# Kernel optimization log

Hardware: AMD Instinct MI355X
Metric: run time of the kernel (lower is better)

Reference implementation:

```python
import jax, jax.numpy as jnp
from jax import lax
import numpy as np

B, N_VARS, M_CLAUSES, K_DIM = 1024, 64, 256, 12
MAX_ITER = 12


def setup_inputs() -> dict:
    key = jax.random.key(0)
    k1, k2, k3, k4 = jax.random.split(key, 4)
    z = jax.random.uniform(k1, (B, N_VARS), dtype=jnp.float32)          # input probabilities
    S = jax.random.normal(k2, (M_CLAUSES, N_VARS + 1), dtype=jnp.float32) * 0.2  # learnable clause matrix (col 0 = truth var)
    w = jax.random.uniform(k3, (M_CLAUSES,), dtype=jnp.float32)          # learnable clause weights
    r = jax.random.normal(k4, (B, N_VARS, K_DIM), dtype=jnp.float32)     # random init directions
    return {"z": z, "S": S, "w": w, "r": r, "max_iter": MAX_ITER}


def _mixing(z, S, w, r, max_iter):
    Bsz, n = z.shape
    m, N = S.shape  # N = n + 1 (truth variable is column 0)
    k = r.shape[-1]
    eps = jnp.float32(1e-8)

    # truth direction v_T = e_0
    vT = jnp.zeros((k,), dtype=z.dtype).at[0].set(1.0)

    # random unit directions orthogonal to v_T (zero out component along e_0)
    r_perp = r.at[..., 0].set(0.0)
    r_perp = r_perp / jnp.maximum(jnp.linalg.norm(r_perp, axis=-1, keepdims=True), eps)

    # SATNet init: v_i = -cos(pi z_i) v_T + sin(pi z_i) r_perp_i
    ang = jnp.pi * z
    Vvars = -jnp.cos(ang)[..., None] * vT + jnp.sin(ang)[..., None] * r_perp  # [B,n,k]
    V = jnp.concatenate([jnp.broadcast_to(vT, (Bsz, 1, k)), Vvars], axis=1)   # [B,N,k]

    Sw = S * w[:, None]                       # weighted clause matrix [m,N]
    W = jnp.einsum('mn,bnk->bmk', Sw, V)      # running product Sw @ V, [B,m,k]
    snrm = jnp.sum(Sw * Sw, axis=0)           # ||s_i||^2 per variable, [N]

    def coord_step(carry, i):
        V, W = carry
        s_i = Sw[:, i]                         # [m]
        v_old = V[:, i, :]                     # [B,k]
        g = jnp.einsum('bmk,m->bk', W, s_i) - snrm[i] * v_old
        v_new = -g / jnp.maximum(jnp.linalg.norm(g, axis=-1, keepdims=True), eps)
        W = W + (v_new - v_old)[:, None, :] * s_i[None, :, None]  # rank-1 update
        V = V.at[:, i, :].set(v_new)
        return (V, W), None

    def sweep(carry, _):
        carry, _ = lax.scan(coord_step, carry, jnp.arange(1, N))  # coordinate descent over variables
        return carry, None

    (V, _), _ = lax.scan(sweep, (V, W), None, length=max_iter)

    # output probabilities: z_i = arccos(-v_i . v_T) / pi
    cos = jnp.clip(-V[:, 1:, 0], -1.0 + 1e-6, 1.0 - 1e-6)
    return jnp.arccos(cos) / jnp.pi


def reference(z, S, w, r, max_iter):
    return _mixing(z, S, w, r, max_iter)
```

## Files before the change

### kernel.cpp

```cpp
#include <hip/hip_runtime.h>
#include <math.h>

#define BATCH 1024
#define NV    64
#define MC    256
#define KD    12
#define PI_F  3.14159265358979323846f

#define CBUF   4544
#define C0OFF  4352
#define DGAOFF 4416
#define DGBOFF 4480

typedef float f2 __attribute__((ext_vector_type(2)));
typedef float v4f __attribute__((ext_vector_type(4)));

template <int CTRL>
__device__ __forceinline__ float dpp_addf(float x) {
  int y = __builtin_amdgcn_update_dpp(0, __float_as_int(x), CTRL, 0xF, 0xF, true);
  return x + __int_as_float(y);
}
__device__ __forceinline__ float allreduce16(float x) {
  x = dpp_addf<0xB1>(x);
  x = dpp_addf<0x4E>(x);
  x = dpp_addf<0x124>(x);
  x = dpp_addf<0x128>(x);
  return x;
}
__device__ __forceinline__ float readlane63(float x) {
  return __int_as_float(__builtin_amdgcn_readlane(__float_as_int(x), 63));
}

__device__ __forceinline__ void pin(v4f& x) { asm volatile("" : "+v"(x)); }

__global__ void compute_C_kernel(const float* __restrict__ S,
                                 const float* __restrict__ w,
                                 float* __restrict__ Cg, int nsplit) {
  const int q = blockIdx.x;
  const int mc = blockIdx.y;
  const int j = threadIdx.x;
  if (j > NV) return;
  const int v = (q + 1) % 64 + 1;
  const int mlen = MC / nsplit;
  const int m0 = mc * mlen;
  float a0 = 0.f, a1 = 0.f, a2 = 0.f, a3 = 0.f;
  for (int m = m0; m < m0 + mlen; m += 4) {
    const float w0 = w[m], w1 = w[m + 1], w2 = w[m + 2], w3 = w[m + 3];
    a0 = fmaf(S[(m + 0) * (NV + 1) + v] * w0 * w0, S[(m + 0) * (NV + 1) + j], a0);
    a1 = fmaf(S[(m + 1) * (NV + 1) + v] * w1 * w1, S[(m + 1) * (NV + 1) + j], a1);
    a2 = fmaf(S[(m + 2) * (NV + 1) + v] * w2 * w2, S[(m + 2) * (NV + 1) + j], a2);
    a3 = fmaf(S[(m + 3) * (NV + 1) + v] * w3 * w3, S[(m + 3) * (NV + 1) + j], a3);
  }
  const float acc = (a0 + a1) + (a2 + a3);
  float* buf = Cg + mc * CBUF;
  const int p1 = (v == 1) ? 64 : (v - 1);
  const int p2 = (v == 1) ? 63 : (v == 2) ? 64 : (v - 2);
  if (j == 0) buf[C0OFF + q] = acc;
  if (j == p1) buf[DGAOFF + (v - 1)] = acc;
  if (j == p2) buf[DGBOFF + (v - 1)] = acc;
  if (j > 0) {
    const float st = (j == v || j == p1 || j == p2) ? 0.f : acc;
    buf[q * 68 + (j - 1)] = st;
  }
}

__global__ __launch_bounds__(256, 1) void mixing_kernel(
    const float* __restrict__ z, const float* __restrict__ r,
    const float* __restrict__ Cg, const int* __restrict__ max_iter_p,
    float* __restrict__ out, int nsplit) {
  __shared__ float Ls[CBUF];

  const int t = threadIdx.x;
  const int l = t & 63;
  const int kq = l >> 4;
  const int n16 = l & 15;
  const int b = blockIdx.x * 4 + (t >> 6);
  const int max_iter = max_iter_p[0];

  {
    const float4* src = (const float4*)Cg;
    float4* dst = (float4*)Ls;
    for (int idx = t; idx < CBUF / 4; idx += 256) {
      float4 a = src[idx];
      for (int u = 1; u < nsplit; ++u) {
        const float4 p = src[u * (CBUF / 4) + idx];
        a.x += p.x; a.y += p.y; a.z += p.z; a.w += p.w;
      }
      dst[idx] = a;
    }
  }

  const float row0 = (kq == 0) ? 1.f : 0.f;

  f2 V01[4];
  float V2[4];
  #pragma unroll
  for (int s = 0; s < 4; ++s) {
    const int n = 4 * n16 + s;
    const float zv = z[b * NV + n];
    float rp[3];
    float ssp = 0.f;
    #pragma unroll
    for (int j = 0; j < 3; ++j) {
      const int k = 3 * kq + j;
      rp[j] = (k == 0) ? 0.f : r[(b * NV + n) * KD + k];
      ssp = fmaf(rp[j], rp[j], ssp);
    }
    ssp += __shfl_xor(ssp, 16, 64);
    ssp += __shfl_xor(ssp, 32, 64);
    const float inv = 1.f / fmaxf(sqrtf(ssp), 1e-8f);
    float sn, cs;
    sincosf(PI_F * zv, &sn, &cs);
    float vv[3];
    #pragma unroll
    for (int j = 0; j < 3; ++j) {
      const int k = 3 * kq + j;
      vv[j] = (k == 0) ? -cs : sn * rp[j] * inv;
    }
    V01[s].x = vv[0];
    V01[s].y = vv[1];
    V2[s] = vv[2];
  }

  __syncthreads();

  f2 P01, vp1_01, vp2_01;
  float P2, vp1_2, vp2_2;

  {
    const v4f ce = *(const v4f*)&Ls[63 * 68 + 4 * n16];
    const float c0 = Ls[C0OFF + 63];
    f2 q01 = ce.x * V01[0];
    float q2 = ce.x * V2[0];
    q01 = __builtin_elementwise_fma((f2){ce.y, ce.y}, V01[1], q01);
    q2 = fmaf(ce.y, V2[1], q2);
    q01 = __builtin_elementwise_fma((f2){ce.z, ce.z}, V01[2], q01);
    q2 = fmaf(ce.z, V2[2], q2);
    q01 = __builtin_elementwise_fma((f2){ce.w, ce.w}, V01[3], q01);
    q2 = fmaf(ce.w, V2[3], q2);
    q01.x = allreduce16(q01.x);
    q01.y = allreduce16(q01.y);
    q2 = allreduce16(q2);
    q01.x = fmaf(row0, c0, q01.x);
    P01 = q01; P2 = q2;
    const int src = l | 15;
    vp1_01.x = __shfl(V01[3].x, src, 64);
    vp1_01.y = __shfl(V01[3].y, src, 64);
    vp1_2    = __shfl(V2[3],    src, 64);
    vp2_01.x = __shfl(V01[2].x, src, 64);
    vp2_01.y = __shfl(V01[2].y, src, 64);
    vp2_2    = __shfl(V2[2],    src, 64);
  }

  v4f cbA[4], cbB[4], c0A, c0B, daA, daB, dbA, dbB;

  auto prefetch = [&](v4f cb[4], v4f& c0b, v4f& dab, v4f& dbb, int g) {
    #pragma unroll
    for (int s = 0; s < 4; ++s) {
      cb[s] = *(const v4f*)&Ls[(4 * g + s) * 68 + 4 * n16];
      pin(cb[s]);
    }
    c0b = *(const v4f*)&Ls[C0OFF + 4 * g];
    dab = *(const v4f*)&Ls[DGAOFF + 4 * g];
    dbb = *(const v4f*)&Ls[DGBOFF + 4 * g];
    pin(c0b); pin(dab); pin(dbb);
  };

  auto do_group = [&](int ii, const v4f cb[4], const v4f& c0b,
                      const v4f& dab, const v4f& dbb) {
    const bool own  = (n16 == ii);
    const bool ownP = (n16 == ((ii + 15) & 15));
    #pragma unroll
    for (int s = 0; s < 4; ++s) {
      const v4f ce = cb[s];
      const float db = dbb[s], da = dab[s];

      f2 g01 = __builtin_elementwise_fma((f2){db, db}, vp2_01, P01);
      float g2 = fmaf(db, vp2_2, P2);
      g01 = __builtin_elementwise_fma((f2){da, da}, vp1_01, g01);
      g2 = fmaf(da, vp1_2, g2);

      f2 q01 = ce.x * V01[0];
      float q2 = ce.x * V2[0];
      q01 = __builtin_elementwise_fma((f2){ce.y, ce.y}, V01[1], q01);
      q2 = fmaf(ce.y, V2[1], q2);
      q01 = __builtin_elementwise_fma((f2){ce.z, ce.z}, V01[2], q01);
      q2 = fmaf(ce.z, V2[2], q2);
      q01 = __builtin_elementwise_fma((f2){ce.w, ce.w}, V01[3], q01);
      q2 = fmaf(ce.w, V2[3], q2);

      float n2p = g01.x * g01.x;
      n2p = fmaf(g01.y, g01.y, n2p);
      n2p = fmaf(g2, g2, n2p);

      n2p = dpp_addf<0x142>(n2p);
      q01.x = dpp_addf<0xB1>(q01.x);
      q01.y = dpp_addf<0xB1>(q01.y);
      q2 = dpp_addf<0xB1>(q2);
      n2p = dpp_addf<0x143>(n2p);
      q01.x = dpp_addf<0x4E>(q01.x);
      q01.y = dpp_addf<0x4E>(q01.y);
      q2 = dpp_addf<0x4E>(q2);
      const float n2 = readlane63(n2p);
      q01.x = dpp_addf<0x124>(q01.x);
      q01.y = dpp_addf<0x124>(q01.y);
      q2 = dpp_addf<0x124>(q2);
      const float inv = __builtin_amdgcn_rsqf(fmaxf(n2, 1e-16f));
      q01.x = dpp_addf<0x128>(q01.x);
      q01.y = dpp_addf<0x128>(q01.y);
      q2 = dpp_addf<0x128>(q2);
      const f2 vn01 = g01 * (f2){-inv, -inv};
      const float vn2 = -g2 * inv;
      q01.x = fmaf(row0, c0b[s], q01.x);

      if (s == 0) {
        V01[3].x = ownP ? vp1_01.x : V01[3].x;
        V01[3].y = ownP ? vp1_01.y : V01[3].y;
        V2[3]    = ownP ? vp1_2    : V2[3];
      } else {
        V01[s - 1].x = own ? vp1_01.x : V01[s - 1].x;
        V01[s - 1].y = own ? vp1_01.y : V01[s - 1].y;
        V2[s - 1]    = own ? vp1_2    : V2[s - 1];
      }

      vp2_01 = vp1_01; vp2_2 = vp1_2;
      vp1_01 = vn01;   vp1_2 = vn2;
      P01 = q01;       P2 = q2;
    }
  };

  prefetch(cbA, c0A, daA, dbA, 0);

  for (int it = 0; it < max_iter; ++it) {
    for (int ih = 0; ih < 8; ++ih) {
      prefetch(cbB, c0B, daB, dbB, 2 * ih + 1);
      do_group(2 * ih, cbA, c0A, daA, dbA);
      prefetch(cbA, c0A, daA, dbA, (2 * ih + 2) & 15);
      do_group(2 * ih + 1, cbB, c0B, daB, dbB);
    }
  }

  {
    const bool l15 = (n16 == 15);
    V01[3].x = l15 ? vp1_01.x : V01[3].x;
    V01[3].y = l15 ? vp1_01.y : V01[3].y;
    V2[3]    = l15 ? vp1_2    : V2[3];
  }

  if (kq == 0) {
    float4 o;
    float* op = &o.x;
    #pragma unroll
    for (int s = 0; s < 4; ++s) {
      float cv = -V01[s].x;
      cv = fminf(fmaxf(cv, -1.f + 1e-6f), 1.f - 1e-6f);
      op[s] = acosf(cv) * (1.f / PI_F);
    }
    ((float4*)(out + b * NV))[n16] = o;
  }
}

extern "C" void kernel_launch(void* const* d_in, const int* in_sizes, int n_in,
                              void* d_out, int out_size, void* d_ws, size_t ws_size,
                              hipStream_t stream) {
  const float* z = (const float*)d_in[0];
  const float* S = (const float*)d_in[1];
  const float* w = (const float*)d_in[2];
  const float* r = (const float*)d_in[3];
  const int* max_iter = (const int*)d_in[4];
  float* Cg = (float*)d_ws;

  const int nsplit = (ws_size >= (size_t)8 * CBUF * 4) ? 8
                   : (ws_size >= (size_t)4 * CBUF * 4) ? 4 : 1;
  compute_C_kernel<<<dim3(NV, nsplit), 128, 0, stream>>>(S, w, Cg, nsplit);
  mixing_kernel<<<BATCH / 4, 256, 0, stream>>>(z, r, Cg, max_iter,
                                               (float*)d_out, nsplit);
}
```

Measured before the change: 166.5 us.

## Remap wave lanes to one k-dim per lane group and unroll variable sweep

Changes the per-wave thread mapping. Each lane now holds one k-dimension (kk) for a quarter of the variables (jg), instead of three k-components for four variables. The C matrix layout in LDS is rearranged to match, and the reduction over variables shrinks to two DPP steps plus one norm reduction across lane groups. The 64-step coordinate sweep is fully unrolled with inline-asm ds_read_b128 prefetches three rows ahead, and the per-step scalars are fetched with readlane from registers. This should cut the VALU and DPP work per step, at the cost of code size and more fragile hand scheduling with manual waitcnt.

```diff
diff --git a/kernel.cpp b/kernel.cpp
--- a/kernel.cpp
+++ b/kernel.cpp
@@ -7,31 +7,36 @@
 #define KD    12
 #define PI_F  3.14159265358979323846f
 
-#define CBUF   4544
-#define C0OFF  4352
-#define DGAOFF 4416
-#define DGBOFF 4480
-
-typedef float f2 __attribute__((ext_vector_type(2)));
+#define C0OFF  4096
+#define DGAOFF 4160
+#define DGBOFF 4224
+#define CBUF   4288
+
+typedef float f2  __attribute__((ext_vector_type(2)));
 typedef float v4f __attribute__((ext_vector_type(4)));
+typedef __attribute__((address_space(3))) float lds_f;
 
 template <int CTRL>
 __device__ __forceinline__ float dpp_addf(float x) {
   int y = __builtin_amdgcn_update_dpp(0, __float_as_int(x), CTRL, 0xF, 0xF, true);
   return x + __int_as_float(y);
 }
-__device__ __forceinline__ float allreduce16(float x) {
-  x = dpp_addf<0xB1>(x);
-  x = dpp_addf<0x4E>(x);
-  x = dpp_addf<0x124>(x);
-  x = dpp_addf<0x128>(x);
-  return x;
+template <int CTRL>
+__device__ __forceinline__ float dpp_movf(float x) {
+  return __int_as_float(
+      __builtin_amdgcn_update_dpp(0, __float_as_int(x), CTRL, 0xF, 0xF, true));
 }
 __device__ __forceinline__ float readlane63(float x) {
   return __int_as_float(__builtin_amdgcn_readlane(__float_as_int(x), 63));
 }
-
-__device__ __forceinline__ void pin(v4f& x) { asm volatile("" : "+v"(x)); }
+__device__ __forceinline__ float rlane(float x, int i) {
+  return __int_as_float(__builtin_amdgcn_readlane(__float_as_int(x), i));
+}
+
+template <int IMM>
+__device__ __forceinline__ void dsr(v4f& d, unsigned base) {
+  asm volatile("ds_read_b128 %0, %1 offset:%2" : "=v"(d) : "v"(base), "i"(IMM));
+}
 
 __global__ void compute_C_kernel(const float* __restrict__ S,
                                  const float* __restrict__ w,
@@ -59,8 +64,9 @@
   if (j == p1) buf[DGAOFF + (v - 1)] = acc;
   if (j == p2) buf[DGBOFF + (v - 1)] = acc;
   if (j > 0) {
+    const int j0 = j - 1;
     const float st = (j == v || j == p1 || j == p2) ? 0.f : acc;
-    buf[q * 68 + (j - 1)] = st;
+    buf[q * 64 + (j0 & 3) * 16 + (j0 >> 2)] = st;
   }
 }
 
@@ -68,12 +74,12 @@
     const float* __restrict__ z, const float* __restrict__ r,
     const float* __restrict__ Cg, const int* __restrict__ max_iter_p,
     float* __restrict__ out, int nsplit) {
-  __shared__ float Ls[CBUF];
+  __shared__ __align__(16) float Ls[CBUF];
 
   const int t = threadIdx.x;
   const int l = t & 63;
-  const int kq = l >> 4;
-  const int n16 = l & 15;
+  const int jg = l & 3;
+  const int kk = l >> 2;
   const int b = blockIdx.x * 4 + (t >> 6);
   const int max_iter = max_iter_p[0];
 
@@ -90,173 +96,143 @@
     }
   }
 
-  const float row0 = (kq == 0) ? 1.f : 0.f;
-
-  f2 V01[4];
-  float V2[4];
+  const float my_e0 = (kk == 0) ? 1.f : 0.f;
+
+  f2 Vv[8];
   #pragma unroll
-  for (int s = 0; s < 4; ++s) {
-    const int n = 4 * n16 + s;
-    const float zv = z[b * NV + n];
-    float rp[3];
-    float ssp = 0.f;
+  for (int p = 0; p < 8; ++p) {
     #pragma unroll
-    for (int j = 0; j < 3; ++j) {
-      const int k = 3 * kq + j;
-      rp[j] = (k == 0) ? 0.f : r[(b * NV + n) * KD + k];
-      ssp = fmaf(rp[j], rp[j], ssp);
+    for (int h = 0; h < 2; ++h) {
+      const int j0 = jg + 8 * p + 4 * h;
+      const float zv = z[b * NV + j0];
+      float rp = 0.f;
+      if (kk >= 1 && kk < KD) rp = r[(b * NV + j0) * KD + kk];
+      float ssp = rp * rp;
+      ssp += __shfl_xor(ssp, 4, 64);
+      ssp += __shfl_xor(ssp, 8, 64);
+      ssp += __shfl_xor(ssp, 16, 64);
+      ssp += __shfl_xor(ssp, 32, 64);
+      const float inv = 1.f / fmaxf(sqrtf(ssp), 1e-8f);
+      const float sn = __builtin_amdgcn_sinf(0.5f * zv);
+      const float cs = __builtin_amdgcn_cosf(0.5f * zv);
+      const float vv = (kk == 0) ? -cs : sn * rp * inv;
+      if (h) Vv[p].y = vv; else Vv[p].x = vv;
     }
-    ssp += __shfl_xor(ssp, 16, 64);
-    ssp += __shfl_xor(ssp, 32, 64);
-    const float inv = 1.f / fmaxf(sqrtf(ssp), 1e-8f);
-    float sn, cs;
-    sincosf(PI_F * zv, &sn, &cs);
-    float vv[3];
-    #pragma unroll
-    for (int j = 0; j < 3; ++j) {
-      const int k = 3 * kq + j;
-      vv[j] = (k == 0) ? -cs : sn * rp[j] * inv;
+  }
+
+  __syncthreads();
+
+  const float t0v = Ls[C0OFF + l];
+  const float t1v = Ls[DGAOFF + l];
+  const float t2v = Ls[DGBOFF + l];
+
+  float P, vp1, vp2;
+
+  {
+    const int rb = 63 * 64 + jg * 16;
+    const v4f c0r = *(const v4f*)&Ls[rb + 0];
+    const v4f c1r = *(const v4f*)&Ls[rb + 4];
+    const v4f c2r = *(const v4f*)&Ls[rb + 8];
+    const v4f c3r = *(const v4f*)&Ls[rb + 12];
+    f2 qa = (f2){c0r.x, c0r.y} * Vv[0];
+    qa = __builtin_elementwise_fma((f2){c0r.z, c0r.w}, Vv[1], qa);
+    qa = __builtin_elementwise_fma((f2){c2r.x, c2r.y}, Vv[4], qa);
+    qa = __builtin_elementwise_fma((f2){c2r.z, c2r.w}, Vv[5], qa);
+    f2 qb = (f2){c1r.x, c1r.y} * Vv[2];
+    qb = __builtin_elementwise_fma((f2){c1r.z, c1r.w}, Vv[3], qb);
+    qb = __builtin_elementwise_fma((f2){c3r.x, c3r.y}, Vv[6], qb);
+    qb = __builtin_elementwise_fma((f2){c3r.z, c3r.w}, Vv[7], qb);
+    const f2 qs = qa + qb;
+    float q = qs.x + qs.y;
+    q = dpp_addf<0xB1>(q);
+    q = dpp_addf<0x4E>(q);
+    q = fmaf(my_e0, Ls[C0OFF + 63], q);
+    P = q;
+    vp1 = dpp_movf<0xFF>(Vv[7].y);
+    vp2 = dpp_movf<0xAA>(Vv[7].y);
+  }
+
+  const unsigned lbase = (unsigned)(unsigned long long)(lds_f*)&Ls[jg * 16];
+
+  v4f Rb[16];
+
+#define PFROW(R) \
+  dsr<((((R) & 63) * 256) + 0)>(Rb[(((R) & 3) * 4) + 0], lbase); \
+  dsr<((((R) & 63) * 256) + 16)>(Rb[(((R) & 3) * 4) + 1], lbase); \
+  dsr<((((R) & 63) * 256) + 32)>(Rb[(((R) & 3) * 4) + 2], lbase); \
+  dsr<((((R) & 63) * 256) + 48)>(Rb[(((R) & 3) * 4) + 3], lbase);
+
+#define STEPF(I) { \
+  constexpr int i_ = (I); \
+  constexpr int j0w_ = (i_ + 63) & 63; \
+  constexpr int p_ = j0w_ >> 3; \
+  constexpr int h_ = (j0w_ >> 2) & 1; \
+  constexpr int jgo_ = j0w_ & 3; \
+  constexpr int s_ = (i_ & 3) * 4; \
+   \
+  asm volatile("s_waitcnt lgkmcnt(8)" ::: "memory"); \
+  __builtin_amdgcn_sched_barrier(0); \
+  PFROW(i_ + 3) \
+  const float da_ = rlane(t1v, i_); \
+  const float db_ = rlane(t2v, i_); \
+  const float c0_ = rlane(t0v, i_); \
+  const float g_ = fmaf(da_, vp1, fmaf(db_, vp2, P)); \
+  float t_ = g_ * g_; \
+  f2 qa_ = (f2){Rb[s_ + 0].x, Rb[s_ + 0].y} * Vv[0]; \
+  qa_ = __builtin_elementwise_fma((f2){Rb[s_ + 0].z, Rb[s_ + 0].w}, Vv[1], qa_); \
+  t_ = dpp_addf<0x124>(t_); \
+  qa_ = __builtin_elementwise_fma((f2){Rb[s_ + 2].x, Rb[s_ + 2].y}, Vv[4], qa_); \
+  qa_ = __builtin_elementwise_fma((f2){Rb[s_ + 2].z, Rb[s_ + 2].w}, Vv[5], qa_); \
+  t_ = dpp_addf<0x128>(t_); \
+  f2 qb_ = (f2){Rb[s_ + 1].x, Rb[s_ + 1].y} * Vv[2]; \
+  qb_ = __builtin_elementwise_fma((f2){Rb[s_ + 1].z, Rb[s_ + 1].w}, Vv[3], qb_); \
+  t_ = dpp_addf<0x142>(t_); \
+  qb_ = __builtin_elementwise_fma((f2){Rb[s_ + 3].x, Rb[s_ + 3].y}, Vv[6], qb_); \
+  qb_ = __builtin_elementwise_fma((f2){Rb[s_ + 3].z, Rb[s_ + 3].w}, Vv[7], qb_); \
+  t_ = dpp_addf<0x143>(t_); \
+  const f2 qs_ = qa_ + qb_; \
+  float q_ = qs_.x + qs_.y; \
+  const float n2_ = readlane63(t_); \
+  const float inv_ = __builtin_amdgcn_rsqf(fmaxf(n2_, 1e-16f)); \
+  q_ = dpp_addf<0xB1>(q_); \
+  q_ = dpp_addf<0x4E>(q_); \
+  const float vn_ = -g_ * inv_; \
+  q_ = fmaf(my_e0, c0_, q_); \
+  if constexpr (h_) { Vv[p_].y = (jg == jgo_) ? vp1 : Vv[p_].y; } \
+  else              { Vv[p_].x = (jg == jgo_) ? vp1 : Vv[p_].x; } \
+  vp2 = vp1; vp1 = vn_; P = q_; \
+}
+
+#define S4(N) STEPF((N) + 0) STEPF((N) + 1) STEPF((N) + 2) STEPF((N) + 3)
+#define S16(N) S4((N) + 0) S4((N) + 4) S4((N) + 8) S4((N) + 12)
+
+  asm volatile("s_waitcnt lgkmcnt(0)" ::: "memory");
+  __builtin_amdgcn_sched_barrier(0);
+  PFROW(0) PFROW(1) PFROW(2)
+
+  #pragma unroll 1
+  for (int it = 0; it < max_iter; ++it) {
+    S16(0) S16(16) S16(32) S16(48)
+  }
+
+  Vv[7].y = (jg == 3) ? vp1 : Vv[7].y;
+
+  __syncthreads();
+  {
+    float* Lw = Ls + (t >> 6) * 64;
+    if (kk == 0) {
+      Lw[jg +  0] = Vv[0].x; Lw[jg +  4] = Vv[0].y;
+      Lw[jg +  8] = Vv[1].x; Lw[jg + 12] = Vv[1].y;
+      Lw[jg + 16] = Vv[2].x; Lw[jg + 20] = Vv[2].y;
+      Lw[jg + 24] = Vv[3].x; Lw[jg + 28] = Vv[3].y;
+      Lw[jg + 32] = Vv[4].x; Lw[jg + 36] = Vv[4].y;
+      Lw[jg + 40] = Vv[5].x; Lw[jg + 44] = Vv[5].y;
+      Lw[jg + 48] = Vv[6].x; Lw[jg + 52] = Vv[6].y;
+      Lw[jg + 56] = Vv[7].x; Lw[jg + 60] = Vv[7].y;
     }
-    V01[s].x = vv[0];
-    V01[s].y = vv[1];
-    V2[s] = vv[2];
-  }
-
-  __syncthreads();
-
-  f2 P01, vp1_01, vp2_01;
-  float P2, vp1_2, vp2_2;
-
-  {
-    const v4f ce = *(const v4f*)&Ls[63 * 68 + 4 * n16];
-    const float c0 = Ls[C0OFF + 63];
-    f2 q01 = ce.x * V01[0];
-    float q2 = ce.x * V2[0];
-    q01 = __builtin_elementwise_fma((f2){ce.y, ce.y}, V01[1], q01);
-    q2 = fmaf(ce.y, V2[1], q2);
-    q01 = __builtin_elementwise_fma((f2){ce.z, ce.z}, V01[2], q01);
-    q2 = fmaf(ce.z, V2[2], q2);
-    q01 = __builtin_elementwise_fma((f2){ce.w, ce.w}, V01[3], q01);
-    q2 = fmaf(ce.w, V2[3], q2);
-    q01.x = allreduce16(q01.x);
-    q01.y = allreduce16(q01.y);
-    q2 = allreduce16(q2);
-    q01.x = fmaf(row0, c0, q01.x);
-    P01 = q01; P2 = q2;
-    const int src = l | 15;
-    vp1_01.x = __shfl(V01[3].x, src, 64);
-    vp1_01.y = __shfl(V01[3].y, src, 64);
-    vp1_2    = __shfl(V2[3],    src, 64);
-    vp2_01.x = __shfl(V01[2].x, src, 64);
-    vp2_01.y = __shfl(V01[2].y, src, 64);
-    vp2_2    = __shfl(V2[2],    src, 64);
-  }
-
-  v4f cbA[4], cbB[4], c0A, c0B, daA, daB, dbA, dbB;
-
-  auto prefetch = [&](v4f cb[4], v4f& c0b, v4f& dab, v4f& dbb, int g) {
-    #pragma unroll
-    for (int s = 0; s < 4; ++s) {
-      cb[s] = *(const v4f*)&Ls[(4 * g + s) * 68 + 4 * n16];
-      pin(cb[s]);
-    }
-    c0b = *(const v4f*)&Ls[C0OFF + 4 * g];
-    dab = *(const v4f*)&Ls[DGAOFF + 4 * g];
-    dbb = *(const v4f*)&Ls[DGBOFF + 4 * g];
-    pin(c0b); pin(dab); pin(dbb);
-  };
-
-  auto do_group = [&](int ii, const v4f cb[4], const v4f& c0b,
-                      const v4f& dab, const v4f& dbb) {
-    const bool own  = (n16 == ii);
-    const bool ownP = (n16 == ((ii + 15) & 15));
-    #pragma unroll
-    for (int s = 0; s < 4; ++s) {
-      const v4f ce = cb[s];
-      const float db = dbb[s], da = dab[s];
-
-      f2 g01 = __builtin_elementwise_fma((f2){db, db}, vp2_01, P01);
-      float g2 = fmaf(db, vp2_2, P2);
-      g01 = __builtin_elementwise_fma((f2){da, da}, vp1_01, g01);
-      g2 = fmaf(da, vp1_2, g2);
-
-      f2 q01 = ce.x * V01[0];
-      float q2 = ce.x * V2[0];
-      q01 = __builtin_elementwise_fma((f2){ce.y, ce.y}, V01[1], q01);
-      q2 = fmaf(ce.y, V2[1], q2);
-      q01 = __builtin_elementwise_fma((f2){ce.z, ce.z}, V01[2], q01);
-      q2 = fmaf(ce.z, V2[2], q2);
-      q01 = __builtin_elementwise_fma((f2){ce.w, ce.w}, V01[3], q01);
-      q2 = fmaf(ce.w, V2[3], q2);
-
-      float n2p = g01.x * g01.x;
-      n2p = fmaf(g01.y, g01.y, n2p);
-      n2p = fmaf(g2, g2, n2p);
-
-      n2p = dpp_addf<0x142>(n2p);
-      q01.x = dpp_addf<0xB1>(q01.x);
-      q01.y = dpp_addf<0xB1>(q01.y);
-      q2 = dpp_addf<0xB1>(q2);
-      n2p = dpp_addf<0x143>(n2p);
-      q01.x = dpp_addf<0x4E>(q01.x);
-      q01.y = dpp_addf<0x4E>(q01.y);
-      q2 = dpp_addf<0x4E>(q2);
-      const float n2 = readlane63(n2p);
-      q01.x = dpp_addf<0x124>(q01.x);
-      q01.y = dpp_addf<0x124>(q01.y);
-      q2 = dpp_addf<0x124>(q2);
-      const float inv = __builtin_amdgcn_rsqf(fmaxf(n2, 1e-16f));
-      q01.x = dpp_addf<0x128>(q01.x);
-      q01.y = dpp_addf<0x128>(q01.y);
-      q2 = dpp_addf<0x128>(q2);
-      const f2 vn01 = g01 * (f2){-inv, -inv};
-      const float vn2 = -g2 * inv;
-      q01.x = fmaf(row0, c0b[s], q01.x);
-
-      if (s == 0) {
-        V01[3].x = ownP ? vp1_01.x : V01[3].x;
-        V01[3].y = ownP ? vp1_01.y : V01[3].y;
-        V2[3]    = ownP ? vp1_2    : V2[3];
-      } else {
-        V01[s - 1].x = own ? vp1_01.x : V01[s - 1].x;
-        V01[s - 1].y = own ? vp1_01.y : V01[s - 1].y;
-        V2[s - 1]    = own ? vp1_2    : V2[s - 1];
-      }
-
-      vp2_01 = vp1_01; vp2_2 = vp1_2;
-      vp1_01 = vn01;   vp1_2 = vn2;
-      P01 = q01;       P2 = q2;
-    }
-  };
-
-  prefetch(cbA, c0A, daA, dbA, 0);
-
-  for (int it = 0; it < max_iter; ++it) {
-    for (int ih = 0; ih < 8; ++ih) {
-      prefetch(cbB, c0B, daB, dbB, 2 * ih + 1);
-      do_group(2 * ih, cbA, c0A, daA, dbA);
-      prefetch(cbA, c0A, daA, dbA, (2 * ih + 2) & 15);
-      do_group(2 * ih + 1, cbB, c0B, daB, dbB);
-    }
-  }
-
-  {
-    const bool l15 = (n16 == 15);
-    V01[3].x = l15 ? vp1_01.x : V01[3].x;
-    V01[3].y = l15 ? vp1_01.y : V01[3].y;
-    V2[3]    = l15 ? vp1_2    : V2[3];
-  }
-
-  if (kq == 0) {
-    float4 o;
-    float* op = &o.x;
-    #pragma unroll
-    for (int s = 0; s < 4; ++s) {
-      float cv = -V01[s].x;
-      cv = fminf(fmaxf(cv, -1.f + 1e-6f), 1.f - 1e-6f);
-      op[s] = acosf(cv) * (1.f / PI_F);
-    }
-    ((float4*)(out + b * NV))[n16] = o;
+    float cv = -Lw[l];
+    cv = fminf(fmaxf(cv, -1.f + 1e-6f), 1.f - 1e-6f);
+    out[b * NV + l] = acosf(cv) * (1.f / PI_F);
   }
 }
 
```

Measured after the change: 145.5 us. -12.6%, faster.
